# Kernel optimization log

Hardware: AMD Instinct MI355X
Metric: run time of the kernel (lower is better)

## Reference

```python
import jax, jax.numpy as jnp
import numpy as np

BATCH = 262144
CLUSTER = 100

def _boost_generators():
    # Standard Lorentz boost generators K_x, K_y, K_z (symmetric, metric (+,-,-,-)).
    K = np.zeros((3, 4, 4), dtype=np.float32)
    for j in range(3):
        K[j, 0, j + 1] = 1.0
        K[j, j + 1, 0] = 1.0
    return jnp.asarray(K)

def setup_inputs() -> dict:
    key = jax.random.key(0)
    k1, k2, k3, k4 = jax.random.split(key, 4)
    T = jax.random.normal(k1, (BATCH, CLUSTER, 4), dtype=jnp.float32)
    # build() initializes boosts/bias uniform[0,1) scaled by 0.33 (|b| < 1 => gamma real)
    Bo = jax.random.uniform(k2, (CLUSTER, 3), dtype=jnp.float32) * 0.33
    Bi = jax.random.uniform(k3, (1, 3), dtype=jnp.float32) * 0.33
    W = jax.random.uniform(k4, (CLUSTER, 1), dtype=jnp.float32)
    K_mats = _boost_generators()
    return {"T": T, "Bo": Bo, "Bi": Bi, "W": W, "K_mats": K_mats}

def _lorentz(x, boosts, K_mats, weights=None):
    # x: (batch, C, 4), boosts: (C, 3) -> (batch, 4)
    mag = jnp.sqrt(jnp.sum(boosts * boosts, axis=1, keepdims=True))  # (C,1)
    n = boosts / mag                                                  # (C,3)
    g = 1.0 / jnp.sqrt(1.0 - mag * mag)                               # (C,1) gamma
    nK = jnp.einsum('cj,jad->cad', n, K_mats)                         # (C,4,4)
    nK2 = jnp.einsum('cab,cbd->cad', nK, nK)                          # (C,4,4)
    B = (jnp.eye(4, dtype=x.dtype)[None]
         - (g * mag)[..., None] * nK
         + (g - 1.0)[..., None] * nK2)                                # (C,4,4)
    if weights is not None:
        B = weights[:, :, None] * B                                   # per-element scalar weight
    # sum over cluster of B_c @ x[:, c]
    return jnp.einsum('cad,bcd->ba', B, x)

def reference(T, Bo, Bi, W, K_mats):
    summed = _lorentz(T, Bo, K_mats, weights=W)            # (batch, 4)
    out = _lorentz(summed[:, None, :], Bi, K_mats)         # (batch, 4)
    return out.reshape(T.shape[0], 1, 4)
```

## Files before the change

kernel.cpp:

```cpp
#include <hip/hip_runtime.h>
#include <math.h>

#define BATCH   262144
#define CLUSTER 100

__device__ inline void boost_mat(float bx, float by, float bz, float B[4][4]) {
    float m2  = bx * bx + by * by + bz * bz;
    float mag = sqrtf(m2);
    float nx = bx / mag, ny = by / mag, nz = bz / mag;
    float g  = 1.0f / sqrtf(1.0f - mag * mag);
    float gm = g * mag;
    float gm1 = g - 1.0f;
    float n[3] = {nx, ny, nz};
    B[0][0] = 1.0f + gm1 * (nx * nx + ny * ny + nz * nz);
    for (int j = 0; j < 3; ++j) {
        B[0][j + 1] = -gm * n[j];
        B[j + 1][0] = -gm * n[j];
    }
    for (int i = 0; i < 3; ++i)
        for (int j = 0; j < 3; ++j)
            B[i + 1][j + 1] = ((i == j) ? 1.0f : 0.0f) + gm1 * n[i] * n[j];
}

__global__ void build_M_kernel(const float* __restrict__ Bo,
                               const float* __restrict__ Bi,
                               const float* __restrict__ W,
                               float* __restrict__ M) {
    int c = threadIdx.x;
    if (c >= CLUSTER) return;

    float BiM[4][4];
    boost_mat(Bi[0], Bi[1], Bi[2], BiM);

    float BoM[4][4];
    boost_mat(Bo[c * 3 + 0], Bo[c * 3 + 1], Bo[c * 3 + 2], BoM);

    float w = W[c];
    for (int a = 0; a < 4; ++a)
        for (int d = 0; d < 4; ++d) {
            float s = 0.0f;
            for (int e = 0; e < 4; ++e)
                s += BiM[a][e] * (w * BoM[e][d]);
            M[c * 16 + a * 4 + d] = s;
        }
}

#define DOT4(mm, vv) ((mm).x*(vv).x + (mm).y*(vv).y + (mm).z*(vv).z + (mm).w*(vv).w)

__global__ __launch_bounds__(256, 4) void lorentz_main_kernel(
        const float* __restrict__ T,
        const float* __restrict__ M,
        float* __restrict__ out) {
    __shared__ float sM[CLUSTER * 16];

    int tid = threadIdx.x;
    for (int i = tid; i < CLUSTER * 4; i += 256)
        ((float4*)sM)[i] = ((const float4*)M)[i];
    __syncthreads();

    int wave = tid >> 6;
    int lane = tid & 63;
    int q  = lane & 3;
    int g  = lane >> 2;
    long long rowBase = (long long)blockIdx.x * 256 + wave * 64 + g * 4;

    const float* T0 = T + rowBase * (CLUSTER * 4);

    float4 a0 = {0.f, 0.f, 0.f, 0.f};
    float4 a1 = a0, a2 = a0, a3 = a0;

    #pragma unroll 2
    for (int t = 0; t < 25; ++t) {
        int c = 4 * t + q;
        float4 v0 = *(const float4*)(T0 +    0 + c * 4);
        float4 v1 = *(const float4*)(T0 +  400 + c * 4);
        float4 v2 = *(const float4*)(T0 +  800 + c * 4);
        float4 v3 = *(const float4*)(T0 + 1200 + c * 4);
        const float4* m = (const float4*)(sM + c * 16);
        float4 m0 = m[0], m1 = m[1], m2 = m[2], m3 = m[3];

        a0.x += DOT4(m0, v0); a0.y += DOT4(m1, v0); a0.z += DOT4(m2, v0); a0.w += DOT4(m3, v0);
        a1.x += DOT4(m0, v1); a1.y += DOT4(m1, v1); a1.z += DOT4(m2, v1); a1.w += DOT4(m3, v1);
        a2.x += DOT4(m0, v2); a2.y += DOT4(m1, v2); a2.z += DOT4(m2, v2); a2.w += DOT4(m3, v2);
        a3.x += DOT4(m0, v3); a3.y += DOT4(m1, v3); a3.z += DOT4(m2, v3); a3.w += DOT4(m3, v3);
    }

    #define RED(f) f += __shfl_xor(f, 1); f += __shfl_xor(f, 2);
    RED(a0.x) RED(a0.y) RED(a0.z) RED(a0.w)
    RED(a1.x) RED(a1.y) RED(a1.z) RED(a1.w)
    RED(a2.x) RED(a2.y) RED(a2.z) RED(a2.w)
    RED(a3.x) RED(a3.y) RED(a3.z) RED(a3.w)
    #undef RED

    float4 o = a0;
    if (q == 1) o = a1;
    if (q == 2) o = a2;
    if (q == 3) o = a3;
    ((float4*)out)[rowBase + q] = o;
}

extern "C" void kernel_launch(void* const* d_in, const int* in_sizes, int n_in,
                              void* d_out, int out_size, void* d_ws, size_t ws_size,
                              hipStream_t stream) {
    const float* T  = (const float*)d_in[0];
    const float* Bo = (const float*)d_in[1];
    const float* Bi = (const float*)d_in[2];
    const float* W  = (const float*)d_in[3];

    float* M = (float*)d_ws;
    float* out = (float*)d_out;

    build_M_kernel<<<1, 128, 0, stream>>>(Bo, Bi, W, M);

    int blocks = BATCH / 256;
    lorentz_main_kernel<<<blocks, 256, 0, stream>>>(T, M, out);
}
```

Baseline: 92.90 us.

## Fuse boost-matrix construction into main kernel and remap lanes to two rows

Removes the separate single-block build kernel: every block now computes the 100 combined 4x4 matrices straight into shared memory, so one launch and its global round trip go away. The work mapping changes from 4 lanes x 4 rows per group to 8 lanes x 2 rows, with a tail for the last 4 clusters, an extra shuffle stage, and 64 rows per block instead of 256. The cost is redundant matrix construction in every one of 4x as many blocks, including sqrt and divide work that delays the start of the streaming loads, and fewer independent loads in flight per thread.

```diff
diff --git a/kernel.cpp b/kernel.cpp
--- a/kernel.cpp
+++ b/kernel.cpp
@@ -22,81 +22,73 @@
             B[i + 1][j + 1] = ((i == j) ? 1.0f : 0.0f) + gm1 * n[i] * n[j];
 }
 
-__global__ void build_M_kernel(const float* __restrict__ Bo,
-                               const float* __restrict__ Bi,
-                               const float* __restrict__ W,
-                               float* __restrict__ M) {
-    int c = threadIdx.x;
-    if (c >= CLUSTER) return;
-
-    float BiM[4][4];
-    boost_mat(Bi[0], Bi[1], Bi[2], BiM);
-
-    float BoM[4][4];
-    boost_mat(Bo[c * 3 + 0], Bo[c * 3 + 1], Bo[c * 3 + 2], BoM);
-
-    float w = W[c];
-    for (int a = 0; a < 4; ++a)
-        for (int d = 0; d < 4; ++d) {
-            float s = 0.0f;
-            for (int e = 0; e < 4; ++e)
-                s += BiM[a][e] * (w * BoM[e][d]);
-            M[c * 16 + a * 4 + d] = s;
-        }
-}
-
 #define DOT4(mm, vv) ((mm).x*(vv).x + (mm).y*(vv).y + (mm).z*(vv).z + (mm).w*(vv).w)
 
-__global__ __launch_bounds__(256, 4) void lorentz_main_kernel(
+__global__ __launch_bounds__(256) void lorentz_fused_kernel(
         const float* __restrict__ T,
-        const float* __restrict__ M,
+        const float* __restrict__ Bo,
+        const float* __restrict__ Bi,
+        const float* __restrict__ W,
         float* __restrict__ out) {
     __shared__ float sM[CLUSTER * 16];
 
     int tid = threadIdx.x;
-    for (int i = tid; i < CLUSTER * 4; i += 256)
-        ((float4*)sM)[i] = ((const float4*)M)[i];
+    if (tid < CLUSTER) {
+        float BiM[4][4], BoM[4][4];
+        boost_mat(Bi[0], Bi[1], Bi[2], BiM);
+        boost_mat(Bo[tid * 3 + 0], Bo[tid * 3 + 1], Bo[tid * 3 + 2], BoM);
+        float w = W[tid];
+        for (int a = 0; a < 4; ++a)
+            for (int d = 0; d < 4; ++d) {
+                float s = 0.0f;
+                for (int e = 0; e < 4; ++e)
+                    s += BiM[a][e] * (w * BoM[e][d]);
+                sM[tid * 16 + a * 4 + d] = s;
+            }
+    }
     __syncthreads();
 
     int wave = tid >> 6;
     int lane = tid & 63;
-    int q  = lane & 3;
-    int g  = lane >> 2;
-    long long rowBase = (long long)blockIdx.x * 256 + wave * 64 + g * 4;
+    int q = lane & 7;
+    int g = lane >> 3;
+    long long base = (long long)blockIdx.x * 64 + wave * 16;
+    long long row0 = base + g;
+    long long row1 = base + g + 8;
 
-    const float* T0 = T + rowBase * (CLUSTER * 4);
+    const float* P0 = T + row0 * (CLUSTER * 4);
+    const float* P1 = T + row1 * (CLUSTER * 4);
 
     float4 a0 = {0.f, 0.f, 0.f, 0.f};
-    float4 a1 = a0, a2 = a0, a3 = a0;
+    float4 a1 = a0;
 
-    #pragma unroll 2
-    for (int t = 0; t < 25; ++t) {
-        int c = 4 * t + q;
-        float4 v0 = *(const float4*)(T0 +    0 + c * 4);
-        float4 v1 = *(const float4*)(T0 +  400 + c * 4);
-        float4 v2 = *(const float4*)(T0 +  800 + c * 4);
-        float4 v3 = *(const float4*)(T0 + 1200 + c * 4);
+    #pragma unroll 4
+    for (int t = 0; t < 12; ++t) {
+        int c = 8 * t + q;
+        float4 v0 = *(const float4*)(P0 + c * 4);
+        float4 v1 = *(const float4*)(P1 + c * 4);
         const float4* m = (const float4*)(sM + c * 16);
         float4 m0 = m[0], m1 = m[1], m2 = m[2], m3 = m[3];
-
         a0.x += DOT4(m0, v0); a0.y += DOT4(m1, v0); a0.z += DOT4(m2, v0); a0.w += DOT4(m3, v0);
         a1.x += DOT4(m0, v1); a1.y += DOT4(m1, v1); a1.z += DOT4(m2, v1); a1.w += DOT4(m3, v1);
-        a2.x += DOT4(m0, v2); a2.y += DOT4(m1, v2); a2.z += DOT4(m2, v2); a2.w += DOT4(m3, v2);
-        a3.x += DOT4(m0, v3); a3.y += DOT4(m1, v3); a3.z += DOT4(m2, v3); a3.w += DOT4(m3, v3);
+    }
+    if (q < 4) {
+        int c = 96 + q;
+        float4 v0 = *(const float4*)(P0 + c * 4);
+        float4 v1 = *(const float4*)(P1 + c * 4);
+        const float4* m = (const float4*)(sM + c * 16);
+        float4 m0 = m[0], m1 = m[1], m2 = m[2], m3 = m[3];
+        a0.x += DOT4(m0, v0); a0.y += DOT4(m1, v0); a0.z += DOT4(m2, v0); a0.w += DOT4(m3, v0);
+        a1.x += DOT4(m0, v1); a1.y += DOT4(m1, v1); a1.z += DOT4(m2, v1); a1.w += DOT4(m3, v1);
     }
 
-    #define RED(f) f += __shfl_xor(f, 1); f += __shfl_xor(f, 2);
+    #define RED(f) f += __shfl_xor(f, 1); f += __shfl_xor(f, 2); f += __shfl_xor(f, 4);
     RED(a0.x) RED(a0.y) RED(a0.z) RED(a0.w)
     RED(a1.x) RED(a1.y) RED(a1.z) RED(a1.w)
-    RED(a2.x) RED(a2.y) RED(a2.z) RED(a2.w)
-    RED(a3.x) RED(a3.y) RED(a3.z) RED(a3.w)
     #undef RED
 
-    float4 o = a0;
-    if (q == 1) o = a1;
-    if (q == 2) o = a2;
-    if (q == 3) o = a3;
-    ((float4*)out)[rowBase + q] = o;
+    if (q == 0) ((float4*)out)[row0] = a0;
+    if (q == 1) ((float4*)out)[row1] = a1;
 }
 
 extern "C" void kernel_launch(void* const* d_in, const int* in_sizes, int n_in,
@@ -107,11 +99,8 @@
     const float* Bi = (const float*)d_in[2];
     const float* W  = (const float*)d_in[3];
 
-    float* M = (float*)d_ws;
     float* out = (float*)d_out;
 
-    build_M_kernel<<<1, 128, 0, stream>>>(Bo, Bi, W, M);
-
-    int blocks = BATCH / 256;
-    lorentz_main_kernel<<<blocks, 256, 0, stream>>>(T, M, out);
+    int blocks = BATCH / 64;
+    lorentz_fused_kernel<<<blocks, 256, 0, stream>>>(T, Bo, Bi, W, out);
 }
```

Result: faster. 77.82 us (median of 2 runs) (-16.2%).
